# Kernel optimization log

Hardware: AMD Instinct MI355X
Metric: run time of the kernel (lower is better)

## Reference

```python
import jax, jax.numpy as jnp
import numpy as np

B, T, I, H, O = 64, 2048, 128, 256, 128
K1 = 1
K2 = 1


def setup_inputs() -> dict:
    key = jax.random.key(0)
    ks = jax.random.split(key, 8)
    M = H - K1 + 1
    return {
        "x": jax.random.normal(ks[0], (B, T, I), jnp.float32),
        "W_in": jax.random.normal(ks[1], (H, I), jnp.float32) / np.sqrt(I).astype(np.float32),
        "b_in": jax.random.normal(ks[2], (H,), jnp.float32) * 0.01,
        "W_out": jax.random.normal(ks[3], (O, H), jnp.float32) / np.sqrt(H).astype(np.float32),
        "b_out": jax.random.normal(ks[4], (O,), jnp.float32) * 0.01,
        # padded Householder vectors: row i uses its first K+i entries (masked in reference)
        # uniform in [0.5, 1.5] keeps u.u well away from 0 (avoids 2/<u,u> blowup)
        "u_raw": jax.random.uniform(ks[5], (M, H), jnp.float32, 0.5, 1.5),
        "sigmas": jnp.ones((H,), jnp.float32),
        "v_raw": jax.random.uniform(ks[6], (M, H), jnp.float32, 0.5, 1.5),
    }


def _householder_chain(hats):
    # U <- H_last @ ... @ H_0, H_i = I - 2/<u,u> u u^T, applied as rank-1 updates
    Hdim = hats.shape[1]
    def step(Umat, u):
        beta = 2.0 / jnp.dot(u, u)
        return Umat - beta * jnp.outer(u, u @ Umat), None
    U, _ = jax.lax.scan(step, jnp.eye(Hdim, dtype=hats.dtype), hats)
    return U


def reference(x, W_in, b_in, W_out, b_out, u_raw, sigmas, v_raw):
    Hdim = sigmas.shape[0]
    Mu = u_raw.shape[0]
    Mv = v_raw.shape[0]
    # row i of u_hats has entries in cols [0, K1+i), then flipped along cols
    mask_u = jnp.arange(Hdim)[None, :] < (K1 + jnp.arange(Mu))[:, None]
    u_hats = jnp.flip(jnp.where(mask_u, u_raw, 0.0), axis=1)
    mask_v = jnp.arange(Hdim)[None, :] < (K2 + jnp.arange(Mv))[:, None]
    v_hats = jnp.flip(jnp.where(mask_v, v_raw, 0.0), axis=(0, 1))  # torch.flip dims=[0,1]
    U = _householder_chain(u_hats)
    V = _householder_chain(v_hats)
    W = (U * sigmas[None, :]) @ V  # U @ diag(sigmas) @ V
    # precompute input projection for all timesteps: [T, B, H]
    xproj = jnp.einsum('bti,hi->tbh', x, W_in) + b_in
    h0 = jnp.zeros((x.shape[0], Hdim), x.dtype)
    def cell(h, xp):
        h = jnp.tanh(xp + h @ W.T)
        return h, h @ W_out.T + b_out
    _, out = jax.lax.scan(cell, h0, xproj)  # out: [T, B, O]
    return jnp.transpose(out, (1, 0, 2))
```

## Files before the change

### kernel.cpp

```cpp
#include <hip/hip_runtime.h>
#include <hip/hip_bf16.h>
#include <hip/hip_fp16.h>

#define BB 64
#define TT 2048
#define II 128
#define HH 256
#define OO 128
#define RCH 8

typedef _Float16 f16x2 __attribute__((ext_vector_type(2)));

#if __has_builtin(__builtin_amdgcn_fdot2)
__device__ __forceinline__ float fdot2(f16x2 a, f16x2 b, float c) {
    return __builtin_amdgcn_fdot2(a, b, c, false);
}
#else
__device__ __forceinline__ float fdot2(f16x2 a, f16x2 b, float c) {
    return fmaf((float)a.x, (float)b.x, fmaf((float)a.y, (float)b.y, c));
}
#endif

__device__ __forceinline__ f16x2 u2h(unsigned int u) { return __builtin_bit_cast(f16x2, u); }
__device__ __forceinline__ unsigned int packf16(float a, float b) {
    return __builtin_bit_cast(unsigned int, f16x2{(_Float16)a, (_Float16)b});
}

__device__ __forceinline__ float tanh_fast(float x) {
    float xc = fminf(fmaxf(x, -9.0f), 9.0f);
    float e = __expf(2.0f * xc);
    return (e - 1.0f) * __fdividef(1.0f, e + 1.0f);
}

__global__ __launch_bounds__(64) void prep_kernel(
    const float* __restrict__ u_raw, const float* __restrict__ v_raw,
    float* __restrict__ u_eff, float* __restrict__ v_eff,
    float* __restrict__ beta_u, float* __restrict__ beta_v)
{
    const int row = blockIdx.x;
    const int lane = threadIdx.x;
    const bool isU = row < HH;
    const int i = isU ? row : row - HH;
    const float* src = isU ? (u_raw + (size_t)i * HH) : (v_raw + (size_t)(HH - 1 - i) * HH);
    float* dst = (isU ? u_eff : v_eff) + (size_t)i * HH;
    const int lo = isU ? (HH - 1 - i) : i;
    float ss = 0.0f;
    for (int c = lane; c < HH; c += 64) {
        float vv = (c >= lo) ? src[HH - 1 - c] : 0.0f;
        dst[c] = vv;
        ss += vv * vv;
    }
    for (int m = 1; m < 64; m <<= 1) ss += __shfl_xor(ss, m, 64);
    if (lane == 0) (isU ? beta_u : beta_v)[i] = 2.0f / ss;
}

__global__ __launch_bounds__(256) void hh_kernel(
    const float* __restrict__ u_eff, const float* __restrict__ v_eff,
    const float* __restrict__ beta_u, const float* __restrict__ beta_v,
    float* __restrict__ Ucol, float* __restrict__ Vrow)
{
    const int wid = blockIdx.x * 4 + (threadIdx.x >> 6);
    const int lane = threadIdx.x & 63;
    const bool isU = wid < HH;
    const int j = isU ? wid : wid - HH;
    const float* eff = isU ? u_eff : v_eff;
    const float* beta = isU ? beta_u : beta_v;

    float cr0 = (j == 4 * lane + 0) ? 1.0f : 0.0f;
    float cr1 = (j == 4 * lane + 1) ? 1.0f : 0.0f;
    float cr2 = (j == 4 * lane + 2) ? 1.0f : 0.0f;
    float cr3 = (j == 4 * lane + 3) ? 1.0f : 0.0f;

    const int i0 = isU ? (HH - 1 - j) : 0;
    for (int i = i0; i < HH; ++i) {
        const float4 v4 = *(const float4*)(eff + (size_t)i * HH + lane * 4);
        float d = v4.x * cr0 + v4.y * cr1 + v4.z * cr2 + v4.w * cr3;
        for (int m = 1; m < 64; m <<= 1) d += __shfl_xor(d, m, 64);
        const float t = beta[i] * d;
        cr0 = fmaf(-t, v4.x, cr0);
        cr1 = fmaf(-t, v4.y, cr1);
        cr2 = fmaf(-t, v4.z, cr2);
        cr3 = fmaf(-t, v4.w, cr3);
    }
    if (isU) {
        *(float4*)(Ucol + (size_t)j * HH + lane * 4) = make_float4(cr0, cr1, cr2, cr3);
    } else {
        Vrow[(size_t)(4 * lane + 0) * HH + j] = cr0;
        Vrow[(size_t)(4 * lane + 1) * HH + j] = cr1;
        Vrow[(size_t)(4 * lane + 2) * HH + j] = cr2;
        Vrow[(size_t)(4 * lane + 3) * HH + j] = cr3;
    }
}

__global__ __launch_bounds__(256) void w_kernel(
    const float* __restrict__ Ucol, const float* __restrict__ Vrow,
    const float* __restrict__ sig, float* __restrict__ Wm)
{
    const int r = blockIdx.x;
    const int c = threadIdx.x;
    float acc = 0.0f;
    #pragma unroll 4
    for (int k = 0; k < HH; ++k) {
        acc = fmaf(Ucol[(size_t)k * HH + r] * sig[k], Vrow[(size_t)k * HH + c], acc);
    }
    Wm[(size_t)r * HH + c] = acc;
}

__device__ __forceinline__ uint4 stage8(const float* p) {
    float4 a = *(const float4*)p;
    float4 b = *(const float4*)(p + 4);
    return make_uint4(packf16(a.x, a.y), packf16(a.z, a.w),
                      packf16(b.x, b.y), packf16(b.z, b.w));
}
__device__ __forceinline__ uint4 stage8(const __half* p) {
    return *(const uint4*)p;
}
__device__ __forceinline__ void storeC(float* p, float v) { *p = v; }
__device__ __forceinline__ void storeC(__half* p, float v) { *p = __float2half_rn(v); }

template <typename AT, typename OT>
__global__ __launch_bounds__(256) void gemm_bias(
    const AT* __restrict__ A, const float* __restrict__ Bm,
    const float* __restrict__ bias, OT* __restrict__ C,
    int M, int N, int K)
{
    __shared__ unsigned int As[64][20];
    __shared__ unsigned int Bs[64][20];
    const int m0 = blockIdx.x * 64;
    const int n0 = blockIdx.y * 64;
    const int tid = threadIdx.x;
    const int lr = tid >> 2;
    const int lc = (tid & 3) << 3;
    const int tm = tid >> 4;
    const int tn = tid & 15;
    float acc[4][4] = {};
    for (int k0 = 0; k0 < K; k0 += 32) {
        *(uint4*)&As[lr][lc >> 1] = stage8(A + (size_t)(m0 + lr) * K + k0 + lc);
        *(uint4*)&Bs[lr][lc >> 1] = stage8(Bm + (size_t)(n0 + lr) * K + k0 + lc);
        __syncthreads();
        #pragma unroll
        for (int k8 = 0; k8 < 4; ++k8) {
            uint4 a4[4], b4[4];
            #pragma unroll
            for (int r = 0; r < 4; ++r) {
                a4[r] = *(const uint4*)&As[tm * 4 + r][k8 * 4];
                b4[r] = *(const uint4*)&Bs[tn + 16 * r][k8 * 4];
            }
            #pragma unroll
            for (int i2 = 0; i2 < 4; ++i2) {
                #pragma unroll
                for (int j2 = 0; j2 < 4; ++j2) {
                    acc[i2][j2] = fdot2(u2h(a4[i2].x), u2h(b4[j2].x), acc[i2][j2]);
                    acc[i2][j2] = fdot2(u2h(a4[i2].y), u2h(b4[j2].y), acc[i2][j2]);
                    acc[i2][j2] = fdot2(u2h(a4[i2].z), u2h(b4[j2].z), acc[i2][j2]);
                    acc[i2][j2] = fdot2(u2h(a4[i2].w), u2h(b4[j2].w), acc[i2][j2]);
                }
            }
        }
        __syncthreads();
    }
    #pragma unroll
    for (int j2 = 0; j2 < 4; ++j2) {
        const int n = n0 + tn + 16 * j2;
        const float bv = bias[n];
        #pragma unroll
        for (int i2 = 0; i2 < 4; ++i2) {
            const int m = m0 + tm * 4 + i2;
            storeC(C + (size_t)m * N + n, acc[i2][j2] + bv);
        }
    }
}

__global__ __launch_bounds__(512) void recur_kernel(
    const float* __restrict__ Wm,
    const __half* __restrict__ xp,
    __half* __restrict__ hall)
{
    const int b = blockIdx.x;
    const int tid = threadIdx.x;
    const int l = tid & 63;
    const int q = tid >> 6;

    __shared__ float ps[8][HH];
    __shared__ unsigned int hbits[2][HH / 2];

    f16x2 w2[4][16];
    #pragma unroll
    for (int r = 0; r < 4; ++r) {
        const float* Wp = Wm + (size_t)(4 * l + r) * HH + q * 32;
        #pragma unroll
        for (int c4 = 0; c4 < 8; ++c4) {
            float4 f = *(const float4*)(Wp + c4 * 4);
            w2[r][c4 * 2 + 0] = f16x2{(_Float16)f.x, (_Float16)f.y};
            w2[r][c4 * 2 + 1] = f16x2{(_Float16)f.z, (_Float16)f.w};
        }
    }
    if (tid < HH / 2) hbits[0][tid] = 0u;
    __syncthreads();

    const unsigned int* xpw = (const unsigned int*)(xp + (size_t)b * TT * HH);
    unsigned int* hw = (unsigned int*)(hall + (size_t)b * TT * HH);

    unsigned int xpcur[RCH], xpnxt[RCH], hst[RCH];
    if (tid < 128) {
        #pragma unroll
        for (int s = 0; s < RCH; ++s) xpcur[s] = xpw[(size_t)s * 128 + tid];
    }

    const int nch = TT / RCH;
    for (int c = 0; c < nch; ++c) {
        #pragma unroll
        for (int s = 0; s < RCH; ++s) {
            const int p = s & 1;
            if (s == 0 && tid < 128 && c + 1 < nch) {
                const unsigned int* xn = xpw + (size_t)(c + 1) * RCH * 128 + tid;
                #pragma unroll
                for (int s2 = 0; s2 < RCH; ++s2) xpnxt[s2] = xn[(size_t)s2 * 128];
            }
            uint4 ha = *(const uint4*)&hbits[p][q * 16 + 0];
            uint4 hc = *(const uint4*)&hbits[p][q * 16 + 4];
            uint4 hd = *(const uint4*)&hbits[p][q * 16 + 8];
            uint4 he = *(const uint4*)&hbits[p][q * 16 + 12];
            f16x2 hv[16] = {
                u2h(ha.x), u2h(ha.y), u2h(ha.z), u2h(ha.w),
                u2h(hc.x), u2h(hc.y), u2h(hc.z), u2h(hc.w),
                u2h(hd.x), u2h(hd.y), u2h(hd.z), u2h(hd.w),
                u2h(he.x), u2h(he.y), u2h(he.z), u2h(he.w)};
            float a0 = 0.f, a1 = 0.f, a2 = 0.f, a3 = 0.f;
            #pragma unroll
            for (int cc = 0; cc < 16; ++cc) {
                a0 = fdot2(w2[0][cc], hv[cc], a0);
                a1 = fdot2(w2[1][cc], hv[cc], a1);
                a2 = fdot2(w2[2][cc], hv[cc], a2);
                a3 = fdot2(w2[3][cc], hv[cc], a3);
            }
            *(float4*)(&ps[q][4 * l]) = make_float4(a0, a1, a2, a3);
            __syncthreads();

            if (tid < 128) {
                float sx = 0.f, sy = 0.f;
                #pragma unroll
                for (int qq = 0; qq < 8; ++qq) {
                    float2 v = *(const float2*)&ps[qq][2 * tid];
                    sx += v.x; sy += v.y;
                }
                f16x2 xv = u2h(xpcur[s]);
                float h0 = tanh_fast(sx + (float)xv.x);
                float h1 = tanh_fast(sy + (float)xv.y);
                unsigned int hb2 = packf16(h0, h1);
                hbits[p ^ 1][tid] = hb2;
                hst[s] = hb2;
            }
            __syncthreads();
        }
        if (tid < 128) {
            unsigned int* hwc = hw + (size_t)c * RCH * 128 + tid;
            #pragma unroll
            for (int s = 0; s < RCH; ++s) hwc[(size_t)s * 128] = hst[s];
            #pragma unroll
            for (int s = 0; s < RCH; ++s) xpcur[s] = xpnxt[s];
        }
    }
}

extern "C" void kernel_launch(void* const* d_in, const int* in_sizes, int n_in,
                              void* d_out, int out_size, void* d_ws, size_t ws_size,
                              hipStream_t stream) {
    const float* x     = (const float*)d_in[0];
    const float* W_in  = (const float*)d_in[1];
    const float* b_in  = (const float*)d_in[2];
    const float* W_out = (const float*)d_in[3];
    const float* b_out = (const float*)d_in[4];
    const float* u_raw = (const float*)d_in[5];
    const float* sig   = (const float*)d_in[6];
    const float* v_raw = (const float*)d_in[7];
    float* out = (float*)d_out;

    char* ws = (char*)d_ws;
    size_t off = 0;
    auto alloc = [&](size_t bytes) -> void* {
        void* p = (void*)(ws + off);
        off += (bytes + 255) & ~((size_t)255);
        return p;
    };
    float* u_eff  = (float*)alloc((size_t)HH * HH * 4);
    float* v_eff  = (float*)alloc((size_t)HH * HH * 4);
    float* beta_u = (float*)alloc((size_t)HH * 4);
    float* beta_v = (float*)alloc((size_t)HH * 4);
    float* Ucol   = (float*)alloc((size_t)HH * HH * 4);
    float* Vrow   = (float*)alloc((size_t)HH * HH * 4);
    float* Wm     = (float*)alloc((size_t)HH * HH * 4);
    __half* xpbuf = (__half*)alloc((size_t)BB * TT * HH * 2);
    __half* hall  = (__half*)alloc((size_t)BB * TT * HH * 2);
    (void)ws_size; (void)in_sizes; (void)n_in; (void)out_size;

    prep_kernel<<<2 * HH, 64, 0, stream>>>(u_raw, v_raw, u_eff, v_eff, beta_u, beta_v);
    hh_kernel<<<(2 * HH) / 4, 256, 0, stream>>>(u_eff, v_eff, beta_u, beta_v, Ucol, Vrow);
    w_kernel<<<HH, HH, 0, stream>>>(Ucol, Vrow, sig, Wm);
    gemm_bias<float, __half>
        <<<dim3((BB * TT) / 64, HH / 64), 256, 0, stream>>>(x, W_in, b_in, xpbuf, BB * TT, HH, II);
    recur_kernel<<<BB, 512, 0, stream>>>(Wm, xpbuf, hall);
    gemm_bias<__half, float>
        <<<dim3((BB * TT) / 64, OO / 64), 256, 0, stream>>>(hall, W_out, b_out, out, BB * TT, OO, HH);
}
```

Before: 1.547 ms.

## Remove second barrier per step by redundantly computing h slice per wave

Each wave now reads the LDS partial sums for the 32 hidden rows matching its own K slice. It reduces them with a cross-half shuffle, applies tanh, and broadcasts the new h values into registers with readlane. This removes the shared hbits buffer and the second __syncthreads per timestep. The ps buffer is double-buffered to avoid write-after-read hazards. The cost is redundant reduction and tanh work across waves, plus 16-bit global loads and stores instead of 32-bit ones.

```diff
diff --git a/kernel.cpp b/kernel.cpp
--- a/kernel.cpp
+++ b/kernel.cpp
@@ -180,9 +180,11 @@
     const int tid = threadIdx.x;
     const int l = tid & 63;
     const int q = tid >> 6;
-
-    __shared__ float ps[8][HH];
-    __shared__ unsigned int hbits[2][HH / 2];
+    const int lr = l & 31;
+    const int half = l >> 5;
+    const int row = 32 * q + lr;
+
+    __shared__ float ps[2][8][HH];
 
     f16x2 w2[4][16];
     #pragma unroll
@@ -195,37 +197,30 @@
             w2[r][c4 * 2 + 1] = f16x2{(_Float16)f.z, (_Float16)f.w};
         }
     }
-    if (tid < HH / 2) hbits[0][tid] = 0u;
-    __syncthreads();
-
-    const unsigned int* xpw = (const unsigned int*)(xp + (size_t)b * TT * HH);
-    unsigned int* hw = (unsigned int*)(hall + (size_t)b * TT * HH);
-
-    unsigned int xpcur[RCH], xpnxt[RCH], hst[RCH];
-    if (tid < 128) {
-        #pragma unroll
-        for (int s = 0; s < RCH; ++s) xpcur[s] = xpw[(size_t)s * 128 + tid];
-    }
+
+    const unsigned short* xpw16 = (const unsigned short*)(xp + (size_t)b * TT * HH);
+    unsigned short* hw16 = (unsigned short*)(hall + (size_t)b * TT * HH);
+
+    unsigned short xpcur[RCH], xpnxt[RCH], hst[RCH];
+    if (half == 0) {
+        #pragma unroll
+        for (int s = 0; s < RCH; ++s) xpcur[s] = xpw16[(size_t)s * HH + row];
+    }
+
+    f16x2 hv[16];
+    #pragma unroll
+    for (int i = 0; i < 16; ++i) hv[i] = f16x2{(_Float16)0.f, (_Float16)0.f};
 
     const int nch = TT / RCH;
     for (int c = 0; c < nch; ++c) {
         #pragma unroll
         for (int s = 0; s < RCH; ++s) {
             const int p = s & 1;
-            if (s == 0 && tid < 128 && c + 1 < nch) {
-                const unsigned int* xn = xpw + (size_t)(c + 1) * RCH * 128 + tid;
+            if (s == 0 && half == 0 && c + 1 < nch) {
+                const unsigned short* xn = xpw16 + (size_t)(c + 1) * RCH * HH + row;
                 #pragma unroll
-                for (int s2 = 0; s2 < RCH; ++s2) xpnxt[s2] = xn[(size_t)s2 * 128];
-            }
-            uint4 ha = *(const uint4*)&hbits[p][q * 16 + 0];
-            uint4 hc = *(const uint4*)&hbits[p][q * 16 + 4];
-            uint4 hd = *(const uint4*)&hbits[p][q * 16 + 8];
-            uint4 he = *(const uint4*)&hbits[p][q * 16 + 12];
-            f16x2 hv[16] = {
-                u2h(ha.x), u2h(ha.y), u2h(ha.z), u2h(ha.w),
-                u2h(hc.x), u2h(hc.y), u2h(hc.z), u2h(hc.w),
-                u2h(hd.x), u2h(hd.y), u2h(hd.z), u2h(hd.w),
-                u2h(he.x), u2h(he.y), u2h(he.z), u2h(he.w)};
+                for (int s2 = 0; s2 < RCH; ++s2) xpnxt[s2] = xn[(size_t)s2 * HH];
+            }
             float a0 = 0.f, a1 = 0.f, a2 = 0.f, a3 = 0.f;
             #pragma unroll
             for (int cc = 0; cc < 16; ++cc) {
@@ -234,29 +229,34 @@
                 a2 = fdot2(w2[2][cc], hv[cc], a2);
                 a3 = fdot2(w2[3][cc], hv[cc], a3);
             }
-            *(float4*)(&ps[q][4 * l]) = make_float4(a0, a1, a2, a3);
+            *(float4*)(&ps[p][q][4 * l]) = make_float4(a0, a1, a2, a3);
             __syncthreads();
 
-            if (tid < 128) {
-                float sx = 0.f, sy = 0.f;
-                #pragma unroll
-                for (int qq = 0; qq < 8; ++qq) {
-                    float2 v = *(const float2*)&ps[qq][2 * tid];
-                    sx += v.x; sy += v.y;
-                }
-                f16x2 xv = u2h(xpcur[s]);
-                float h0 = tanh_fast(sx + (float)xv.x);
-                float h1 = tanh_fast(sy + (float)xv.y);
-                unsigned int hb2 = packf16(h0, h1);
-                hbits[p ^ 1][tid] = hb2;
-                hst[s] = hb2;
-            }
-            __syncthreads();
-        }
-        if (tid < 128) {
-            unsigned int* hwc = hw + (size_t)c * RCH * 128 + tid;
-            #pragma unroll
-            for (int s = 0; s < RCH; ++s) hwc[(size_t)s * 128] = hst[s];
+            const float* pb = &ps[p][4 * half][row];
+            float r0 = pb[0 * HH], r1 = pb[1 * HH], r2 = pb[2 * HH], r3 = pb[3 * HH];
+            float s4 = (r0 + r1) + (r2 + r3);
+            float tot = s4 + __shfl_xor(s4, 32, 64);
+            float xv = 0.f;
+            if (half == 0) {
+                __half_raw hr; hr.x = xpcur[s];
+                xv = (float)(*(const _Float16*)&hr.x);
+            }
+            float hn = tanh_fast(tot + xv);
+            if (half == 0) {
+                f16x2 t2{(_Float16)hn, (_Float16)0.f};
+                hst[s] = (unsigned short)(__builtin_bit_cast(unsigned int, t2) & 0xffffu);
+            }
+            float hn1 = __shfl_down(hn, 1, 64);
+            unsigned int packed = packf16(hn, hn1);
+            #pragma unroll
+            for (int i = 0; i < 16; ++i) {
+                hv[i] = u2h((unsigned int)__builtin_amdgcn_readlane(packed, 2 * i));
+            }
+        }
+        if (half == 0) {
+            unsigned short* hwc = hw16 + (size_t)c * RCH * HH + row;
+            #pragma unroll
+            for (int s = 0; s < RCH; ++s) hwc[(size_t)s * HH] = hst[s];
             #pragma unroll
             for (int s = 0; s < RCH; ++s) xpcur[s] = xpnxt[s];
         }
```

Result: slower. 1.595 ms (+3.1%).

## Replace fdot2 tiled GEMMs with MFMA 16x16x32 f16 matrix-core GEMM

Applied to the files above, without the earlier changes.

Rewrites the input- and output-projection GEMMs to use the MFMA f32_16x16x32_f16 instruction. Tiles grow to 128x64, each wave computes a 64x32 subtile, and the LDS layout becomes padded f16 rows. The aim is to move the projection arithmetic off scalar dot2 instructions onto matrix cores. The total runtime still includes the sequential recurrence kernel, which this change does not touch, so the overall effect depends on how much of the time the GEMMs take.

```diff
diff --git a/kernel.cpp b/kernel.cpp
--- a/kernel.cpp
+++ b/kernel.cpp
@@ -10,6 +10,8 @@
 #define RCH 8
 
 typedef _Float16 f16x2 __attribute__((ext_vector_type(2)));
+typedef _Float16 f16x8 __attribute__((ext_vector_type(8)));
+typedef float f32x4 __attribute__((ext_vector_type(4)));
 
 #if __has_builtin(__builtin_amdgcn_fdot2)
 __device__ __forceinline__ float fdot2(f16x2 a, f16x2 b, float c) {
@@ -106,67 +108,72 @@
     Wm[(size_t)r * HH + c] = acc;
 }
 
-__device__ __forceinline__ uint4 stage8(const float* p) {
-    float4 a = *(const float4*)p;
-    float4 b = *(const float4*)(p + 4);
-    return make_uint4(packf16(a.x, a.y), packf16(a.z, a.w),
-                      packf16(b.x, b.y), packf16(b.z, b.w));
-}
-__device__ __forceinline__ uint4 stage8(const __half* p) {
-    return *(const uint4*)p;
+__device__ __forceinline__ void stage16(_Float16* dst, const float* src) {
+    #pragma unroll
+    for (int i = 0; i < 4; ++i) {
+        float4 f = ((const float4*)src)[i];
+        ((f16x2*)dst)[2 * i + 0] = f16x2{(_Float16)f.x, (_Float16)f.y};
+        ((f16x2*)dst)[2 * i + 1] = f16x2{(_Float16)f.z, (_Float16)f.w};
+    }
+}
+__device__ __forceinline__ void stage16(_Float16* dst, const __half* src) {
+    ((uint4*)dst)[0] = ((const uint4*)src)[0];
+    ((uint4*)dst)[1] = ((const uint4*)src)[1];
 }
 __device__ __forceinline__ void storeC(float* p, float v) { *p = v; }
 __device__ __forceinline__ void storeC(__half* p, float v) { *p = __float2half_rn(v); }
 
 template <typename AT, typename OT>
-__global__ __launch_bounds__(256) void gemm_bias(
+__global__ __launch_bounds__(256) void gemm_mfma(
     const AT* __restrict__ A, const float* __restrict__ Bm,
     const float* __restrict__ bias, OT* __restrict__ C,
     int M, int N, int K)
 {
-    __shared__ unsigned int As[64][20];
-    __shared__ unsigned int Bs[64][20];
-    const int m0 = blockIdx.x * 64;
+    __shared__ _Float16 As[128][40];
+    __shared__ _Float16 Bs[64][40];
+    const int tid = threadIdx.x;
+    const int m0 = blockIdx.x * 128;
     const int n0 = blockIdx.y * 64;
-    const int tid = threadIdx.x;
-    const int lr = tid >> 2;
-    const int lc = (tid & 3) << 3;
-    const int tm = tid >> 4;
-    const int tn = tid & 15;
-    float acc[4][4] = {};
+    const int lane = tid & 63;
+    const int w = tid >> 6;
+    const int lo = lane & 15;
+    const int qd = lane >> 4;
+    const int mh = w >> 1;
+    const int nh = w & 1;
+    const int srow = tid >> 1;
+    const int shalf = tid & 1;
+
+    f32x4 acc[4][2] = {};
     for (int k0 = 0; k0 < K; k0 += 32) {
-        *(uint4*)&As[lr][lc >> 1] = stage8(A + (size_t)(m0 + lr) * K + k0 + lc);
-        *(uint4*)&Bs[lr][lc >> 1] = stage8(Bm + (size_t)(n0 + lr) * K + k0 + lc);
+        stage16(&As[srow][shalf * 16], A + (size_t)(m0 + srow) * K + k0 + shalf * 16);
+        if (tid < 128)
+            stage16(&Bs[srow][shalf * 16], Bm + (size_t)(n0 + srow) * K + k0 + shalf * 16);
         __syncthreads();
-        #pragma unroll
-        for (int k8 = 0; k8 < 4; ++k8) {
-            uint4 a4[4], b4[4];
-            #pragma unroll
-            for (int r = 0; r < 4; ++r) {
-                a4[r] = *(const uint4*)&As[tm * 4 + r][k8 * 4];
-                b4[r] = *(const uint4*)&Bs[tn + 16 * r][k8 * 4];
-            }
-            #pragma unroll
-            for (int i2 = 0; i2 < 4; ++i2) {
-                #pragma unroll
-                for (int j2 = 0; j2 < 4; ++j2) {
-                    acc[i2][j2] = fdot2(u2h(a4[i2].x), u2h(b4[j2].x), acc[i2][j2]);
-                    acc[i2][j2] = fdot2(u2h(a4[i2].y), u2h(b4[j2].y), acc[i2][j2]);
-                    acc[i2][j2] = fdot2(u2h(a4[i2].z), u2h(b4[j2].z), acc[i2][j2]);
-                    acc[i2][j2] = fdot2(u2h(a4[i2].w), u2h(b4[j2].w), acc[i2][j2]);
-                }
-            }
-        }
+        f16x8 af[4], bf[2];
+        #pragma unroll
+        for (int mt = 0; mt < 4; ++mt)
+            af[mt] = *(const f16x8*)&As[64 * mh + 16 * mt + lo][qd * 8];
+        #pragma unroll
+        for (int nt = 0; nt < 2; ++nt)
+            bf[nt] = *(const f16x8*)&Bs[32 * nh + 16 * nt + lo][qd * 8];
+        #pragma unroll
+        for (int mt = 0; mt < 4; ++mt)
+            #pragma unroll
+            for (int nt = 0; nt < 2; ++nt)
+                acc[mt][nt] = __builtin_amdgcn_mfma_f32_16x16x32_f16(
+                    af[mt], bf[nt], acc[mt][nt], 0, 0, 0);
         __syncthreads();
     }
     #pragma unroll
-    for (int j2 = 0; j2 < 4; ++j2) {
-        const int n = n0 + tn + 16 * j2;
+    for (int nt = 0; nt < 2; ++nt) {
+        const int n = n0 + 32 * nh + 16 * nt + lo;
         const float bv = bias[n];
         #pragma unroll
-        for (int i2 = 0; i2 < 4; ++i2) {
-            const int m = m0 + tm * 4 + i2;
-            storeC(C + (size_t)m * N + n, acc[i2][j2] + bv);
+        for (int mt = 0; mt < 4; ++mt) {
+            const int m = m0 + 64 * mh + 16 * mt + 4 * qd;
+            #pragma unroll
+            for (int r = 0; r < 4; ++r)
+                storeC(C + (size_t)(m + r) * N + n, acc[mt][nt][r] + bv);
         }
     }
 }
@@ -297,9 +304,9 @@
     prep_kernel<<<2 * HH, 64, 0, stream>>>(u_raw, v_raw, u_eff, v_eff, beta_u, beta_v);
     hh_kernel<<<(2 * HH) / 4, 256, 0, stream>>>(u_eff, v_eff, beta_u, beta_v, Ucol, Vrow);
     w_kernel<<<HH, HH, 0, stream>>>(Ucol, Vrow, sig, Wm);
-    gemm_bias<float, __half>
-        <<<dim3((BB * TT) / 64, HH / 64), 256, 0, stream>>>(x, W_in, b_in, xpbuf, BB * TT, HH, II);
+    gemm_mfma<float, __half>
+        <<<dim3((BB * TT) / 128, HH / 64), 256, 0, stream>>>(x, W_in, b_in, xpbuf, BB * TT, HH, II);
     recur_kernel<<<BB, 512, 0, stream>>>(Wm, xpbuf, hall);
-    gemm_bias<__half, float>
-        <<<dim3((BB * TT) / 64, OO / 64), 256, 0, stream>>>(hall, W_out, b_out, out, BB * TT, OO, HH);
-}
+    gemm_mfma<__half, float>
+        <<<dim3((BB * TT) / 128, OO / 64), 256, 0, stream>>>(hall, W_out, b_out, out, BB * TT, OO, HH);
+}
```

After: 1.504 ms. 2.8% less time.
